# Kernel optimization log

Measured on AMD Instinct MI355X. Metric: run time of the kernel, lower is better.

## Reference

```python
import jax, jax.numpy as jnp
import numpy as np

B, N1, N2, D = 4, 4096, 4096, 128


def setup_inputs() -> dict:
    key = jax.random.key(0)
    k1, k2 = jax.random.split(key)
    x1 = jax.random.normal(k1, (B, N1, D), dtype=jnp.float32)
    x2 = jax.random.normal(k2, (B, N2, D), dtype=jnp.float32)
    return {"x1": x1, "x2": x2}


def reference(x1, x2):
    # torch.cdist(x2, x1, p=2.0): pairwise euclidean distances [B, N2, N1]
    # Expansion form: ||a||^2 + ||b||^2 - 2 a.b  (single GEMM, no [B,N2,N1,D] intermediate)
    sq2 = jnp.sum(x2 * x2, axis=-1)                      # [B, N2]
    sq1 = jnp.sum(x1 * x1, axis=-1)                      # [B, N1]
    inner = jnp.einsum('bnd,bmd->bnm', x2, x1)           # [B, N2, N1]
    sq = sq2[:, :, None] + sq1[:, None, :] - 2.0 * inner
    corr_mat = jnp.sqrt(jnp.maximum(sq, 0.0))            # clamp numerical negatives
    max_ind21 = jnp.argmin(corr_mat, axis=-1)            # [B, N2] nearest x1 for each x2
    max_ind12 = jnp.argmin(corr_mat, axis=-2)            # [B, N1] nearest x2 for each x1
    return (x1, x2, corr_mat, max_ind12, max_ind21)
```

## Files before the change

kernel.cpp:

```cpp
#include <hip/hip_runtime.h>
#include <stdint.h>
#include <stddef.h>

#define BB 4
#define NN 4096
#define DD 128

typedef _Float16 f16;
typedef _Float16 f16x8 __attribute__((ext_vector_type(8)));
typedef float f32x4 __attribute__((ext_vector_type(4)));

__device__ __forceinline__ void gl16(const f16* g, f16* l) {
  __builtin_amdgcn_global_load_lds(
      (const __attribute__((address_space(1))) unsigned int*)g,
      (__attribute__((address_space(3))) unsigned int*)l,
      16, 0, 0);
}

__global__ __launch_bounds__(256) void prep_kernel(
    const float* __restrict__ x1, const float* __restrict__ x2,
    f16* __restrict__ x1h, f16* __restrict__ x1l,
    f16* __restrict__ x2h, f16* __restrict__ x2l,
    float* __restrict__ sq1, float* __restrict__ sq2,
    float* __restrict__ out)
{
  int gtid = blockIdx.x * blockDim.x + threadIdx.x;
  int gwave = gtid >> 6;
  int lane = gtid & 63;
  int sub = lane >> 3;
  int j = lane & 7;
  int row = gwave * 8 + sub;
  const float* src; f16* dh; f16* dl; float* sq; float* cpy; int r;
  if (row < BB * NN) {
    r = row; src = x1; dh = x1h; dl = x1l; sq = sq1; cpy = out;
  } else {
    r = row - BB * NN; src = x2; dh = x2h; dl = x2l; sq = sq2;
    cpy = out + (size_t)BB * NN * DD;
  }
  const float* p = src + (size_t)r * DD;
  float acc = 0.0f;
  #pragma unroll
  for (int i = 0; i < DD / 8; ++i) {
    int c = j + i * 8;
    float v = p[c];
    float s = v * v;
    acc = (i == 0) ? s : (acc + s);
    f16 h = (f16)v;
    f16 l = (f16)(v - (float)h);
    dh[(size_t)r * DD + c] = h;
    dl[(size_t)r * DD + c] = l;
    cpy[(size_t)r * DD + c] = v;
  }
  acc = acc + __shfl_xor(acc, 1);
  acc = acc + __shfl_xor(acc, 2);
  acc = acc + __shfl_xor(acc, 4);
  if (j == 0) sq[r] = acc;
}

__global__ __launch_bounds__(256) void cdist_kernel(
    const f16* __restrict__ x2h, const f16* __restrict__ x2l,
    const f16* __restrict__ x1h, const f16* __restrict__ x1l,
    const float* __restrict__ sq2, const float* __restrict__ sq1,
    float* __restrict__ corr,
    float* __restrict__ p21v, int* __restrict__ p21i,
    float* __restrict__ p12v, int* __restrict__ p12i)
{
  __shared__ f16 Ah[128 * 32];
  __shared__ f16 Al[128 * 32];
  __shared__ f16 Bh[128 * 32];
  __shared__ f16 Bl[128 * 32];
  __shared__ float s2s[128];
  __shared__ float s1s[128];

  const int b = blockIdx.z;
  const int bn1 = blockIdx.x * 128;
  const int bn2 = blockIdx.y * 128;
  const int t = threadIdx.x;
  const int wid = t >> 6;
  const int lane = t & 63;
  const int wm = wid >> 1;
  const int wn = wid & 1;
  const int lr = lane & 15;
  const int lg = lane >> 4;

  const f16* gAh = x2h + (size_t)b * NN * DD;
  const f16* gAl = x2l + (size_t)b * NN * DD;
  const f16* gBh = x1h + (size_t)b * NN * DD;
  const f16* gBl = x1l + (size_t)b * NN * DD;

  if (t < 128) s2s[t] = sq2[(size_t)b * NN + bn2 + t];
  else         s1s[t - 128] = sq1[(size_t)b * NN + bn1 + (t - 128)];

  f32x4 acc[4][4];
  #pragma unroll
  for (int m = 0; m < 4; ++m)
    #pragma unroll
    for (int n = 0; n < 4; ++n)
      #pragma unroll
      for (int q = 0; q < 4; ++q) acc[m][n][q] = 0.0f;

  for (int k0 = 0; k0 < DD; k0 += 32) {
    {
      const int cb = wid * 128;
      #pragma unroll
      for (int i = 0; i < 2; ++i) {
        const int c = cb + i * 64 + lane;
        const int rowc = c >> 2;
        const int koff = (c & 3) * 8;
        const int loff = (cb + i * 64) * 8;
        const size_t ga = (size_t)(bn2 + rowc) * DD + k0 + koff;
        const size_t gb = (size_t)(bn1 + rowc) * DD + k0 + koff;
        gl16(gAh + ga, &Ah[loff]);
        gl16(gAl + ga, &Al[loff]);
        gl16(gBh + gb, &Bh[loff]);
        gl16(gBl + gb, &Bl[loff]);
      }
    }
    __syncthreads();

    f16x8 fah[4], fal[4], fbh[4], fbl[4];
    #pragma unroll
    for (int m = 0; m < 4; ++m) {
      const int off = (wm * 64 + m * 16 + lr) * 32 + lg * 8;
      fah[m] = *(const f16x8*)&Ah[off];
      fal[m] = *(const f16x8*)&Al[off];
    }
    #pragma unroll
    for (int n = 0; n < 4; ++n) {
      const int off = (wn * 64 + n * 16 + lr) * 32 + lg * 8;
      fbh[n] = *(const f16x8*)&Bh[off];
      fbl[n] = *(const f16x8*)&Bl[off];
    }
    #pragma unroll
    for (int m = 0; m < 4; ++m)
      #pragma unroll
      for (int n = 0; n < 4; ++n) {
        acc[m][n] = __builtin_amdgcn_mfma_f32_16x16x32_f16(fah[m], fbh[n], acc[m][n], 0, 0, 0);
        acc[m][n] = __builtin_amdgcn_mfma_f32_16x16x32_f16(fah[m], fbl[n], acc[m][n], 0, 0, 0);
        acc[m][n] = __builtin_amdgcn_mfma_f32_16x16x32_f16(fal[m], fbh[n], acc[m][n], 0, 0, 0);
      }
    __syncthreads();
  }

  float bv21[4][4]; int bi21[4][4];
  float bv12[4];    int bi12[4];
  #pragma unroll
  for (int m = 0; m < 4; ++m)
    #pragma unroll
    for (int q = 0; q < 4; ++q) { bv21[m][q] = 3.4e38f; bi21[m][q] = 0; }
  #pragma unroll
  for (int n = 0; n < 4; ++n) { bv12[n] = 3.4e38f; bi12[n] = 0; }

  float* cbase = corr + (size_t)b * NN * NN;
  #pragma unroll
  for (int m = 0; m < 4; ++m) {
    #pragma unroll
    for (int n = 0; n < 4; ++n) {
      #pragma unroll
      for (int q = 0; q < 4; ++q) {
        const int rl = wm * 64 + m * 16 + lg * 4 + q;
        const int cl = wn * 64 + n * 16 + lr;
        const float inner = acc[m][n][q];
        const float sqv = (s2s[rl] + s1s[cl]) - 2.0f * inner;
        const float dist = sqrtf(fmaxf(sqv, 0.0f));
        cbase[(size_t)(bn2 + rl) * NN + (bn1 + cl)] = dist;
        if (dist < bv21[m][q]) { bv21[m][q] = dist; bi21[m][q] = bn1 + cl; }
        if (dist < bv12[n])    { bv12[n] = dist;    bi12[n] = bn2 + rl; }
      }
    }
  }

  #pragma unroll
  for (int m = 0; m < 4; ++m)
    #pragma unroll
    for (int q = 0; q < 4; ++q) {
      float v = bv21[m][q]; int idx = bi21[m][q];
      #pragma unroll
      for (int mask = 1; mask < 16; mask <<= 1) {
        float ov = __shfl_xor(v, mask);
        int oi = __shfl_xor(idx, mask);
        if (ov < v || (ov == v && oi < idx)) { v = ov; idx = oi; }
      }
      if (lr == 0) {
        const int rowg = bn2 + wm * 64 + m * 16 + lg * 4 + q;
        const size_t o = ((size_t)b * NN + rowg) * 64 + (blockIdx.x * 2 + wn);
        p21v[o] = v; p21i[o] = idx;
      }
    }
  #pragma unroll
  for (int n = 0; n < 4; ++n) {
    float v = bv12[n]; int idx = bi12[n];
    #pragma unroll
    for (int mask = 16; mask < 64; mask <<= 1) {
      float ov = __shfl_xor(v, mask);
      int oi = __shfl_xor(idx, mask);
      if (ov < v || (ov == v && oi < idx)) { v = ov; idx = oi; }
    }
    if (lg == 0) {
      const int colg = bn1 + wn * 64 + n * 16 + lr;
      const size_t o = ((size_t)b * NN + colg) * 64 + (blockIdx.y * 2 + wm);
      p12v[o] = v; p12i[o] = idx;
    }
  }
}

__global__ __launch_bounds__(256) void argmin_reduce_kernel(
    const float* __restrict__ p21v, const int* __restrict__ p21i,
    const float* __restrict__ p12v, const int* __restrict__ p12i,
    float* __restrict__ out_i12, float* __restrict__ out_i21)
{
  int gtid = blockIdx.x * blockDim.x + threadIdx.x;
  int gwave = gtid >> 6;
  int lane = gtid & 63;
  const float* pv; const int* pi; float* dst; int r;
  if (gwave < BB * NN) { r = gwave; pv = p21v; pi = p21i; dst = out_i21; }
  else { r = gwave - BB * NN; pv = p12v; pi = p12i; dst = out_i12; }
  float v = pv[(size_t)r * 64 + lane];
  int idx = pi[(size_t)r * 64 + lane];
  #pragma unroll
  for (int mask = 1; mask < 64; mask <<= 1) {
    float ov = __shfl_xor(v, mask);
    int oi = __shfl_xor(idx, mask);
    if (ov < v || (ov == v && oi < idx)) { v = ov; idx = oi; }
  }
  if (lane == 0) dst[r] = (float)idx;
}

extern "C" void kernel_launch(void* const* d_in, const int* in_sizes, int n_in,
                              void* d_out, int out_size, void* d_ws, size_t ws_size,
                              hipStream_t stream) {
  (void)in_sizes; (void)n_in; (void)out_size; (void)ws_size;
  const float* x1 = (const float*)d_in[0];
  const float* x2 = (const float*)d_in[1];
  float* out = (float*)d_out;
  char* ws = (char*)d_ws;
  const size_t nd = (size_t)BB * NN * DD;

  f16* x1h = (f16*)(ws + 0 * nd * 2);
  f16* x1l = (f16*)(ws + 1 * nd * 2);
  f16* x2h = (f16*)(ws + 2 * nd * 2);
  f16* x2l = (f16*)(ws + 3 * nd * 2);
  float* sq1 = (float*)(ws + 4 * nd * 2);
  float* sq2 = (float*)(ws + 4 * nd * 2 + (size_t)BB * NN * 4);
  char* pbase = ws + 4 * nd * 2 + 2 * (size_t)BB * NN * 4;
  float* p21v = (float*)(pbase + 0 * (size_t)BB * NN * 64 * 4);
  int*   p21i = (int*)  (pbase + 1 * (size_t)BB * NN * 64 * 4);
  float* p12v = (float*)(pbase + 2 * (size_t)BB * NN * 64 * 4);
  int*   p12i = (int*)  (pbase + 3 * (size_t)BB * NN * 64 * 4);

  hipLaunchKernelGGL(prep_kernel, dim3(1024), dim3(256), 0, stream,
                     x1, x2, x1h, x1l, x2h, x2l, sq1, sq2, out);

  float* corr = out + 2 * nd;
  hipLaunchKernelGGL(cdist_kernel, dim3(32, 32, 4), dim3(256), 0, stream,
                     x2h, x2l, x1h, x1l, sq2, sq1, corr, p21v, p21i, p12v, p12i);

  float* out_i12 = out + 2 * nd + (size_t)BB * NN * NN;
  float* out_i21 = out_i12 + (size_t)BB * NN;
  hipLaunchKernelGGL(argmin_reduce_kernel, dim3(8192), dim3(256), 0, stream,
                     p21v, p21i, p12v, p12i, out_i12, out_i21);
}
```

Baseline: 185.7 us.

## Swap GEMM operands for vector stores, swizzle LDS, prefetch next k-slice

Swaps the GEMM operand roles so each lane's four accumulator values are contiguous along the output row, which allows one 16-byte vector store per fragment to the large distance matrix instead of scalar stores. An XOR swizzle is applied to the LDS layout to avoid bank conflicts on fragment reads. The next k-slice is issued into LDS right after the fragments are read into registers, so the global-to-LDS load overlaps the MFMAs. The argmin tracking now compares squared distances rather than square roots and preloads the norms into registers. This adds an extra barrier per iteration and relies on the swizzle matching between the writer and reader index maps.

```diff
diff --git a/kernel.cpp b/kernel.cpp
--- a/kernel.cpp
+++ b/kernel.cpp
@@ -58,9 +58,9 @@
 }
 
 __global__ __launch_bounds__(256) void cdist_kernel(
+    const f16* __restrict__ x1h, const f16* __restrict__ x1l,
     const f16* __restrict__ x2h, const f16* __restrict__ x2l,
-    const f16* __restrict__ x1h, const f16* __restrict__ x1l,
-    const float* __restrict__ sq2, const float* __restrict__ sq1,
+    const float* __restrict__ sq1, const float* __restrict__ sq2,
     float* __restrict__ corr,
     float* __restrict__ p21v, int* __restrict__ p21i,
     float* __restrict__ p12v, int* __restrict__ p12i)
@@ -69,8 +69,8 @@
   __shared__ f16 Al[128 * 32];
   __shared__ f16 Bh[128 * 32];
   __shared__ f16 Bl[128 * 32];
+  __shared__ float s1s[128];
   __shared__ float s2s[128];
-  __shared__ float s1s[128];
 
   const int b = blockIdx.z;
   const int bn1 = blockIdx.x * 128;
@@ -83,13 +83,31 @@
   const int lr = lane & 15;
   const int lg = lane >> 4;
 
-  const f16* gAh = x2h + (size_t)b * NN * DD;
-  const f16* gAl = x2l + (size_t)b * NN * DD;
-  const f16* gBh = x1h + (size_t)b * NN * DD;
-  const f16* gBl = x1l + (size_t)b * NN * DD;
-
-  if (t < 128) s2s[t] = sq2[(size_t)b * NN + bn2 + t];
-  else         s1s[t - 128] = sq1[(size_t)b * NN + bn1 + (t - 128)];
+  const f16* gAh = x1h + (size_t)b * NN * DD;
+  const f16* gAl = x1l + (size_t)b * NN * DD;
+  const f16* gBh = x2h + (size_t)b * NN * DD;
+  const f16* gBl = x2l + (size_t)b * NN * DD;
+
+  if (t < 128) s1s[t] = sq1[(size_t)b * NN + bn1 + t];
+  else         s2s[t - 128] = sq2[(size_t)b * NN + bn2 + (t - 128)];
+
+  int goff_[2], loff_[2];
+  #pragma unroll
+  for (int i = 0; i < 2; ++i) {
+    const int c = wid * 128 + i * 64 + lane;
+    const int rowc = c >> 2;
+    const int kc = (c & 3) ^ (rowc & 3) ^ ((rowc >> 2) & 3);
+    goff_[i] = rowc * DD + kc * 8;
+    loff_[i] = (wid * 128 + i * 64) * 8;
+  }
+#define STAGE(k0) do { \
+    _Pragma("unroll") \
+    for (int i = 0; i < 2; ++i) { \
+      gl16(gAh + (bn1 * DD + goff_[i] + (k0)), &Ah[loff_[i]]); \
+      gl16(gAl + (bn1 * DD + goff_[i] + (k0)), &Al[loff_[i]]); \
+      gl16(gBh + (bn2 * DD + goff_[i] + (k0)), &Bh[loff_[i]]); \
+      gl16(gBl + (bn2 * DD + goff_[i] + (k0)), &Bl[loff_[i]]); \
+    } } while (0)
 
   f32x4 acc[4][4];
   #pragma unroll
@@ -99,38 +117,29 @@
       #pragma unroll
       for (int q = 0; q < 4; ++q) acc[m][n][q] = 0.0f;
 
-  for (int k0 = 0; k0 < DD; k0 += 32) {
-    {
-      const int cb = wid * 128;
-      #pragma unroll
-      for (int i = 0; i < 2; ++i) {
-        const int c = cb + i * 64 + lane;
-        const int rowc = c >> 2;
-        const int koff = (c & 3) * 8;
-        const int loff = (cb + i * 64) * 8;
-        const size_t ga = (size_t)(bn2 + rowc) * DD + k0 + koff;
-        const size_t gb = (size_t)(bn1 + rowc) * DD + k0 + koff;
-        gl16(gAh + ga, &Ah[loff]);
-        gl16(gAl + ga, &Al[loff]);
-        gl16(gBh + gb, &Bh[loff]);
-        gl16(gBl + gb, &Bl[loff]);
-      }
-    }
+  STAGE(0);
+
+  const int lgx8 = (lg ^ (lr & 3) ^ ((lr >> 2) & 3)) * 8;
+  const int offA0 = (wm * 64 + lr) * 32 + lgx8;
+  const int offB0 = (wn * 64 + lr) * 32 + lgx8;
+
+  for (int it = 0; it < 4; ++it) {
     __syncthreads();
-
     f16x8 fah[4], fal[4], fbh[4], fbl[4];
     #pragma unroll
     for (int m = 0; m < 4; ++m) {
-      const int off = (wm * 64 + m * 16 + lr) * 32 + lg * 8;
+      const int off = offA0 + m * (16 * 32);
       fah[m] = *(const f16x8*)&Ah[off];
       fal[m] = *(const f16x8*)&Al[off];
     }
     #pragma unroll
     for (int n = 0; n < 4; ++n) {
-      const int off = (wn * 64 + n * 16 + lr) * 32 + lg * 8;
+      const int off = offB0 + n * (16 * 32);
       fbh[n] = *(const f16x8*)&Bh[off];
       fbl[n] = *(const f16x8*)&Bl[off];
     }
+    __syncthreads();
+    if (it < 3) STAGE((it + 1) * 32);
     #pragma unroll
     for (int m = 0; m < 4; ++m)
       #pragma unroll
@@ -139,42 +148,50 @@
         acc[m][n] = __builtin_amdgcn_mfma_f32_16x16x32_f16(fah[m], fbl[n], acc[m][n], 0, 0, 0);
         acc[m][n] = __builtin_amdgcn_mfma_f32_16x16x32_f16(fal[m], fbh[n], acc[m][n], 0, 0, 0);
       }
-    __syncthreads();
-  }
-
-  float bv21[4][4]; int bi21[4][4];
-  float bv12[4];    int bi12[4];
+  }
+#undef STAGE
+
+  float s2r[4];
+  #pragma unroll
+  for (int n = 0; n < 4; ++n) s2r[n] = s2s[wn * 64 + n * 16 + lr];
+  float s1r[4][4];
   #pragma unroll
   for (int m = 0; m < 4; ++m)
     #pragma unroll
-    for (int q = 0; q < 4; ++q) { bv21[m][q] = 3.4e38f; bi21[m][q] = 0; }
-  #pragma unroll
-  for (int n = 0; n < 4; ++n) { bv12[n] = 3.4e38f; bi12[n] = 0; }
-
-  float* cbase = corr + (size_t)b * NN * NN;
+    for (int q = 0; q < 4; ++q) s1r[m][q] = s1s[wm * 64 + m * 16 + lg * 4 + q];
+
+  float v21[4]; int i21[4];
+  #pragma unroll
+  for (int n = 0; n < 4; ++n) { v21[n] = 3.4e38f; i21[n] = 0; }
+
+  float* cbp = corr + (size_t)b * NN * NN;
   #pragma unroll
   for (int m = 0; m < 4; ++m) {
+    const int n1b = wm * 64 + m * 16 + lg * 4;
+    float v12[4]; int i12[4];
+    #pragma unroll
+    for (int q = 0; q < 4; ++q) { v12[q] = 3.4e38f; i12[q] = 0; }
     #pragma unroll
     for (int n = 0; n < 4; ++n) {
+      const int n2l = wn * 64 + n * 16 + lr;
+      f32x4 dv;
+      float sqc[4];
       #pragma unroll
       for (int q = 0; q < 4; ++q) {
-        const int rl = wm * 64 + m * 16 + lg * 4 + q;
-        const int cl = wn * 64 + n * 16 + lr;
-        const float inner = acc[m][n][q];
-        const float sqv = (s2s[rl] + s1s[cl]) - 2.0f * inner;
-        const float dist = sqrtf(fmaxf(sqv, 0.0f));
-        cbase[(size_t)(bn2 + rl) * NN + (bn1 + cl)] = dist;
-        if (dist < bv21[m][q]) { bv21[m][q] = dist; bi21[m][q] = bn1 + cl; }
-        if (dist < bv12[n])    { bv12[n] = dist;    bi12[n] = bn2 + rl; }
-      }
-    }
-  }
-
-  #pragma unroll
-  for (int m = 0; m < 4; ++m)
+        const float sv = fmaxf(fmaf(-2.0f, acc[m][n][q], s1r[m][q] + s2r[n]), 0.0f);
+        sqc[q] = sv;
+        dv[q] = sqrtf(sv);
+      }
+      *(f32x4*)(cbp + (size_t)(bn2 + n2l) * NN + (bn1 + n1b)) = dv;
+      #pragma unroll
+      for (int q = 0; q < 4; ++q) {
+        if (sqc[q] < v21[n]) { v21[n] = sqc[q]; i21[n] = bn1 + n1b + q; }
+        if (sqc[q] < v12[q]) { v12[q] = sqc[q]; i12[q] = bn2 + n2l; }
+      }
+    }
     #pragma unroll
     for (int q = 0; q < 4; ++q) {
-      float v = bv21[m][q]; int idx = bi21[m][q];
+      float v = v12[q]; int idx = i12[q];
       #pragma unroll
       for (int mask = 1; mask < 16; mask <<= 1) {
         float ov = __shfl_xor(v, mask);
@@ -182,14 +199,15 @@
         if (ov < v || (ov == v && oi < idx)) { v = ov; idx = oi; }
       }
       if (lr == 0) {
-        const int rowg = bn2 + wm * 64 + m * 16 + lg * 4 + q;
-        const size_t o = ((size_t)b * NN + rowg) * 64 + (blockIdx.x * 2 + wn);
-        p21v[o] = v; p21i[o] = idx;
-      }
-    }
+        const int colg = bn1 + n1b + q;
+        const size_t o = ((size_t)b * NN + colg) * 64 + (blockIdx.y * 2 + wn);
+        p12v[o] = v; p12i[o] = idx;
+      }
+    }
+  }
   #pragma unroll
   for (int n = 0; n < 4; ++n) {
-    float v = bv12[n]; int idx = bi12[n];
+    float v = v21[n]; int idx = i21[n];
     #pragma unroll
     for (int mask = 16; mask < 64; mask <<= 1) {
       float ov = __shfl_xor(v, mask);
@@ -197,9 +215,9 @@
       if (ov < v || (ov == v && oi < idx)) { v = ov; idx = oi; }
     }
     if (lg == 0) {
-      const int colg = bn1 + wn * 64 + n * 16 + lr;
-      const size_t o = ((size_t)b * NN + colg) * 64 + (blockIdx.y * 2 + wm);
-      p12v[o] = v; p12i[o] = idx;
+      const int rowg = bn2 + wn * 64 + n * 16 + lr;
+      const size_t o = ((size_t)b * NN + rowg) * 64 + (blockIdx.x * 2 + wm);
+      p21v[o] = v; p21i[o] = idx;
     }
   }
 }
@@ -253,7 +271,7 @@
 
   float* corr = out + 2 * nd;
   hipLaunchKernelGGL(cdist_kernel, dim3(32, 32, 4), dim3(256), 0, stream,
-                     x2h, x2l, x1h, x1l, sq2, sq1, corr, p21v, p21i, p12v, p12i);
+                     x1h, x1l, x2h, x2l, sq1, sq2, corr, p21v, p21i, p12v, p12i);
 
   float* out_i12 = out + 2 * nd + (size_t)BB * NN * NN;
   float* out_i21 = out_i12 + (size_t)BB * NN;
```

New measurement: 179.8 us. 3.2% less time.
